# Kernel tuning notes

Hardware: AMD Instinct MI355X
Metric: run time of the kernel (lower is better)

The kernel has to match this reference:

```python
import jax, jax.numpy as jnp
import numpy as np

EPS_SQRT = 1e-9
EPS_NORM = 1e-12


def setup_inputs() -> dict:
    key = jax.random.key(0)
    k1, k2 = jax.random.split(key)
    shape = (32, 112, 112, 128)  # B, H, W, C
    left = jax.random.normal(k1, shape, dtype=jnp.float32)
    right = jax.random.normal(k2, shape, dtype=jnp.float32)
    return {"left": left, "right": right}


def reference(left, right):
    B, H, W, C = left.shape
    # reshape to [B, H*W, C] and contract over the spatial dim -> [B, C, C]
    l = left.reshape(B, H * W, C)
    r = right.reshape(B, H * W, C)
    dotted = jnp.einsum('bxc,bxd->bcd', l, r)  # batched outer-product pooling
    flat = dotted.reshape(B, C * C)
    # signed square root
    sqrted = jnp.sign(flat) * jnp.sqrt(jnp.abs(flat) + EPS_SQRT)
    # L2 normalize over the flattened bilinear vector (tf.math.l2_normalize)
    sumsq = jnp.sum(jnp.square(sqrted), axis=-1, keepdims=True)
    normed = sqrted * jax.lax.rsqrt(jnp.maximum(sumsq, EPS_NORM))
    return normed
```

## Files before the change

kernel.cpp:

```cpp
#include <hip/hip_runtime.h>
#include <hip/hip_bf16.h>


#define NK      16
#define KC      784
#define KSTEPS  49
#define BATCH   32
#define CDIM    128
#define XDIM    12544

typedef __bf16 bf16x8 __attribute__((ext_vector_type(8)));
typedef float  f32x16 __attribute__((ext_vector_type(16)));
typedef float  f32x4  __attribute__((ext_vector_type(4)));

__device__ float g_part[(size_t)NK * BATCH * CDIM * CDIM];
__device__ float g_ssq[BATCH * 8];

__global__ __launch_bounds__(512, 4)
void bcnn_gemm_kernel(const float* __restrict__ L, const float* __restrict__ R) {
  const int chunk = blockIdx.x;
  const int b     = blockIdx.y;
  const int t     = threadIdx.x;
  const int l     = t & 63;
  const int w     = t >> 6;
  const int wr    = w >> 2;
  const int wc    = w & 3;
  const int lc    = l & 31;
  const int h     = l >> 5;

  __shared__ __bf16 at_hi[2048];
  __shared__ __bf16 at_lo[2048];
  __shared__ __bf16 bt_hi[2048];
  __shared__ __bf16 bt_lo[2048];

  const int trow = t >> 5;
  const int tc4  = (t & 31) << 2;
  const int fx   = t & 7;
  const int hh   = trow >> 3;
  const int klow = trow & 7;

  int eoff[4];
#pragma unroll
  for (int j = 0; j < 4; ++j)
    eoff[j] = (((tc4 << 1) + (((j << 1) + hh) ^ fx)) << 3) + klow;

  const size_t gbase = ((size_t)b * XDIM + (size_t)chunk * KC + trow) * CDIM + tc4;
  const float* Lp = L + gbase;
  const float* Rp = R + gbase;

  const int cA0 = wr * 64 + lc;
  const int cA1 = cA0 + 32;
  const int dB  = wc * 32 + lc;
  const int offA0 = ((2 * cA0 + h) ^ ((cA0 >> 2) & 7)) << 3;
  const int offA1 = ((2 * cA1 + h) ^ ((cA1 >> 2) & 7)) << 3;
  const int offB  = ((2 * dB  + h) ^ ((dB  >> 2) & 7)) << 3;

  f32x16 acc0 = {};
  f32x16 acc1 = {};

  f32x4 lv = *(const f32x4*)Lp;
  f32x4 rv = *(const f32x4*)Rp;

  for (int s = 0; s < KSTEPS; ++s) {
    Lp += 16 * CDIM;
    Rp += 16 * CDIM;
    const float* Lpn = (s < KSTEPS - 1) ? Lp : L;
    const float* Rpn = (s < KSTEPS - 1) ? Rp : R;
    f32x4 lvn = *(const f32x4*)Lpn;
    f32x4 rvn = *(const f32x4*)Rpn;

    __syncthreads();
#pragma unroll
    for (int j = 0; j < 4; ++j) {
      float fl = lv[j];
      __bf16 lh = (__bf16)fl;
      __bf16 ll = (__bf16)(fl - (float)lh);
      at_hi[eoff[j]] = lh;
      at_lo[eoff[j]] = ll;
      float fr = rv[j];
      __bf16 rh = (__bf16)fr;
      __bf16 rl = (__bf16)(fr - (float)rh);
      bt_hi[eoff[j]] = rh;
      bt_lo[eoff[j]] = rl;
    }
    __syncthreads();

    bf16x8 ah0 = *(bf16x8*)&at_hi[offA0];
    bf16x8 al0 = *(bf16x8*)&at_lo[offA0];
    bf16x8 ah1 = *(bf16x8*)&at_hi[offA1];
    bf16x8 al1 = *(bf16x8*)&at_lo[offA1];
    bf16x8 bh  = *(bf16x8*)&bt_hi[offB];
    bf16x8 bl  = *(bf16x8*)&bt_lo[offB];

    acc0 = __builtin_amdgcn_mfma_f32_32x32x16_bf16(ah0, bh, acc0, 0, 0, 0);
    acc1 = __builtin_amdgcn_mfma_f32_32x32x16_bf16(ah1, bh, acc1, 0, 0, 0);
    acc0 = __builtin_amdgcn_mfma_f32_32x32x16_bf16(ah0, bl, acc0, 0, 0, 0);
    acc1 = __builtin_amdgcn_mfma_f32_32x32x16_bf16(ah1, bl, acc1, 0, 0, 0);
    acc0 = __builtin_amdgcn_mfma_f32_32x32x16_bf16(al0, bh, acc0, 0, 0, 0);
    acc1 = __builtin_amdgcn_mfma_f32_32x32x16_bf16(al1, bh, acc1, 0, 0, 0);

    lv = lvn;
    rv = rvn;
  }

  float* outp = g_part + (((size_t)chunk * BATCH + b) << 14);
#pragma unroll
  for (int r = 0; r < 16; ++r) {
    const int row = (r & 3) + ((r >> 2) << 3) + (h << 2);
    outp[(size_t)(wr * 64 + row) * CDIM + (wc * 32 + lc)]      = acc0[r];
    outp[(size_t)(wr * 64 + 32 + row) * CDIM + (wc * 32 + lc)] = acc1[r];
  }
}

__global__ void bcnn_sqrt_kernel(float* __restrict__ out) {
  const int b   = blockIdx.y;
  const int seg = blockIdx.x;
  const int t   = threadIdx.x;
  const int base = seg * 2048;

  float s[8];
  float ss = 0.f;
#pragma unroll
  for (int j = 0; j < 8; ++j) {
    const int idx = base + t + (j << 8);
    float v = 0.f;
#pragma unroll
    for (int ch = 0; ch < NK; ++ch)
      v += g_part[(((size_t)ch * BATCH + b) << 14) + idx];
    float a  = sqrtf(fabsf(v) + 1e-9f);
    float sg = (v > 0.f) ? 1.f : ((v < 0.f) ? -1.f : 0.f);
    float sv = sg * a;
    s[j] = sv;
    ss += sv * sv;
    out[((size_t)b << 14) + idx] = sv;
  }

#pragma unroll
  for (int o = 32; o > 0; o >>= 1) ss += __shfl_down(ss, o, 64);
  __shared__ float red[4];
  const int lane = t & 63, wid = t >> 6;
  if (lane == 0) red[wid] = ss;
  __syncthreads();
  if (t == 0) g_ssq[b * 8 + seg] = red[0] + red[1] + red[2] + red[3];
}

__global__ void bcnn_scale_kernel(float* __restrict__ out) {
  const int b   = blockIdx.y;
  const int seg = blockIdx.x;
  const int t   = threadIdx.x;

  float tot = 0.f;
#pragma unroll
  for (int i = 0; i < 8; ++i) tot += g_ssq[b * 8 + i];
  const float scale = rsqrtf(fmaxf(tot, 1e-12f));

  const size_t base = ((size_t)b << 14) + seg * 2048 + t;
#pragma unroll
  for (int j = 0; j < 8; ++j) out[base + ((size_t)j << 8)] *= scale;
}

extern "C" void kernel_launch(void* const* d_in, const int* in_sizes, int n_in,
                              void* d_out, int out_size, void* d_ws, size_t ws_size,
                              hipStream_t stream) {
  const float* L = (const float*)d_in[0];
  const float* R = (const float*)d_in[1];
  float* out = (float*)d_out;

  dim3 g1(NK, BATCH);
  bcnn_gemm_kernel<<<g1, 512, 0, stream>>>(L, R);

  dim3 g2(8, BATCH);
  bcnn_sqrt_kernel<<<g2, 256, 0, stream>>>(out);
  bcnn_scale_kernel<<<g2, 256, 0, stream>>>(out);
}
```

Before: 99.24 us.

## Deepen GEMM K-tile to 32, repack hi/lo split, increase split-K, vectorize epilogue

The GEMM kernel now processes 32 rows of the spatial dimension per barrier pair instead of 16. It splits the spatial dimension into 28 chunks instead of 16. Each thread loads 8 strided floats and packs the bf16 hi/lo pairs with integer rounding and byte-perm into 128-bit shared stores under a new swizzle. The goal is to halve the barriers and shared-store instructions per MFMA and to raise block count across CUs. In exchange the occupancy hint drops, more per-thread registers are used, and the partial buffer grows, so the reduction kernel reads more data. The reduction and scale kernels are changed to float4 accesses over 16 segments per batch.

```diff
diff --git a/kernel.cpp b/kernel.cpp
--- a/kernel.cpp
+++ b/kernel.cpp
@@ -2,21 +2,41 @@
 #include <hip/hip_bf16.h>
 
 
-#define NK      16
-#define KC      784
-#define KSTEPS  49
+#define NK      28
+#define KC      448
+#define BK      32
+#define NSTEP   14
 #define BATCH   32
 #define CDIM    128
 #define XDIM    12544
 
 typedef __bf16 bf16x8 __attribute__((ext_vector_type(8)));
 typedef float  f32x16 __attribute__((ext_vector_type(16)));
-typedef float  f32x4  __attribute__((ext_vector_type(4)));
 
 __device__ float g_part[(size_t)NK * BATCH * CDIM * CDIM];
-__device__ float g_ssq[BATCH * 8];
+__device__ float g_ssq[BATCH * 16];
 
-__global__ __launch_bounds__(512, 4)
+__device__ __forceinline__ void split_pack(const float* f, uint4& hi, uint4& lo) {
+  uint xh[8]; uint xl[8];
+#pragma unroll
+  for (int i = 0; i < 8; ++i) {
+    uint u = __float_as_uint(f[i]);
+    uint r = u + 0x7FFFu + ((u >> 16) & 1u);
+    xh[i] = r;
+    float hif = __uint_as_float(r & 0xFFFF0000u);
+    xl[i] = __float_as_uint(f[i] - hif);
+  }
+  hi.x = __builtin_amdgcn_perm(xh[1], xh[0], 0x07060302u);
+  hi.y = __builtin_amdgcn_perm(xh[3], xh[2], 0x07060302u);
+  hi.z = __builtin_amdgcn_perm(xh[5], xh[4], 0x07060302u);
+  hi.w = __builtin_amdgcn_perm(xh[7], xh[6], 0x07060302u);
+  lo.x = __builtin_amdgcn_perm(xl[1], xl[0], 0x07060302u);
+  lo.y = __builtin_amdgcn_perm(xl[3], xl[2], 0x07060302u);
+  lo.z = __builtin_amdgcn_perm(xl[5], xl[4], 0x07060302u);
+  lo.w = __builtin_amdgcn_perm(xl[7], xl[6], 0x07060302u);
+}
+
+__global__ __launch_bounds__(512, 2)
 void bcnn_gemm_kernel(const float* __restrict__ L, const float* __restrict__ R) {
   const int chunk = blockIdx.x;
   const int b     = blockIdx.y;
@@ -26,87 +46,72 @@
   const int wr    = w >> 2;
   const int wc    = w & 3;
   const int lc    = l & 31;
-  const int h     = l >> 5;
+  const int hh    = l >> 5;
 
-  __shared__ __bf16 at_hi[2048];
-  __shared__ __bf16 at_lo[2048];
-  __shared__ __bf16 bt_hi[2048];
-  __shared__ __bf16 bt_lo[2048];
+  __shared__ uint4 sAhi[512];
+  __shared__ uint4 sAlo[512];
+  __shared__ uint4 sBhi[512];
+  __shared__ uint4 sBlo[512];
 
-  const int trow = t >> 5;
-  const int tc4  = (t & 31) << 2;
-  const int fx   = t & 7;
-  const int hh   = trow >> 3;
-  const int klow = trow & 7;
+  const int sc = t & 127;
+  const int sh = t >> 7;
+  const int wu = ((sc << 2) + sh) ^ ((sc >> 1) & 7);
 
-  int eoff[4];
-#pragma unroll
-  for (int j = 0; j < 4; ++j)
-    eoff[j] = (((tc4 << 1) + (((j << 1) + hh) ^ fx)) << 3) + klow;
-
-  const size_t gbase = ((size_t)b * XDIM + (size_t)chunk * KC + trow) * CDIM + tc4;
-  const float* Lp = L + gbase;
-  const float* Rp = R + gbase;
+  const size_t gofs = ((size_t)b * XDIM + (size_t)chunk * KC + sh * 8) * CDIM + sc;
+  const float* Lp = L + gofs;
+  const float* Rp = R + gofs;
 
   const int cA0 = wr * 64 + lc;
   const int cA1 = cA0 + 32;
   const int dB  = wc * 32 + lc;
-  const int offA0 = ((2 * cA0 + h) ^ ((cA0 >> 2) & 7)) << 3;
-  const int offA1 = ((2 * cA1 + h) ^ ((cA1 >> 2) & 7)) << 3;
-  const int offB  = ((2 * dB  + h) ^ ((dB  >> 2) & 7)) << 3;
+  const int uA0 = ((cA0 << 2) + hh) ^ ((cA0 >> 1) & 7);
+  const int uA1 = ((cA1 << 2) + hh) ^ ((cA1 >> 1) & 7);
+  const int uB  = ((dB  << 2) + hh) ^ ((dB  >> 1) & 7);
 
   f32x16 acc0 = {};
   f32x16 acc1 = {};
 
-  f32x4 lv = *(const f32x4*)Lp;
-  f32x4 rv = *(const f32x4*)Rp;
+  float fl[8], fr[8];
+#pragma unroll
+  for (int i = 0; i < 8; ++i) { fl[i] = Lp[i * CDIM]; fr[i] = Rp[i * CDIM]; }
 
-  for (int s = 0; s < KSTEPS; ++s) {
-    Lp += 16 * CDIM;
-    Rp += 16 * CDIM;
-    const float* Lpn = (s < KSTEPS - 1) ? Lp : L;
-    const float* Rpn = (s < KSTEPS - 1) ? Rp : R;
-    f32x4 lvn = *(const f32x4*)Lpn;
-    f32x4 rvn = *(const f32x4*)Rpn;
+  for (int s = 0; s < NSTEP; ++s) {
+    __syncthreads();
+    uint4 h4, l4;
+    split_pack(fl, h4, l4);
+    sAhi[wu] = h4; sAlo[wu] = l4;
+    split_pack(fr, h4, l4);
+    sBhi[wu] = h4; sBlo[wu] = l4;
+
+    Lp = (s + 1 < NSTEP) ? Lp + BK * CDIM : L;
+    Rp = (s + 1 < NSTEP) ? Rp + BK * CDIM : R;
+#pragma unroll
+    for (int i = 0; i < 8; ++i) { fl[i] = Lp[i * CDIM]; fr[i] = Rp[i * CDIM]; }
 
     __syncthreads();
+
 #pragma unroll
-    for (int j = 0; j < 4; ++j) {
-      float fl = lv[j];
-      __bf16 lh = (__bf16)fl;
-      __bf16 ll = (__bf16)(fl - (float)lh);
-      at_hi[eoff[j]] = lh;
-      at_lo[eoff[j]] = ll;
-      float fr = rv[j];
-      __bf16 rh = (__bf16)fr;
-      __bf16 rl = (__bf16)(fr - (float)rh);
-      bt_hi[eoff[j]] = rh;
-      bt_lo[eoff[j]] = rl;
+    for (int ss = 0; ss < 2; ++ss) {
+      const int x = ss << 1;
+      bf16x8 ah0 = *(const bf16x8*)&sAhi[uA0 ^ x];
+      bf16x8 al0 = *(const bf16x8*)&sAlo[uA0 ^ x];
+      bf16x8 ah1 = *(const bf16x8*)&sAhi[uA1 ^ x];
+      bf16x8 al1 = *(const bf16x8*)&sAlo[uA1 ^ x];
+      bf16x8 bh  = *(const bf16x8*)&sBhi[uB  ^ x];
+      bf16x8 bl  = *(const bf16x8*)&sBlo[uB  ^ x];
+      acc0 = __builtin_amdgcn_mfma_f32_32x32x16_bf16(ah0, bh, acc0, 0, 0, 0);
+      acc1 = __builtin_amdgcn_mfma_f32_32x32x16_bf16(ah1, bh, acc1, 0, 0, 0);
+      acc0 = __builtin_amdgcn_mfma_f32_32x32x16_bf16(ah0, bl, acc0, 0, 0, 0);
+      acc1 = __builtin_amdgcn_mfma_f32_32x32x16_bf16(ah1, bl, acc1, 0, 0, 0);
+      acc0 = __builtin_amdgcn_mfma_f32_32x32x16_bf16(al0, bh, acc0, 0, 0, 0);
+      acc1 = __builtin_amdgcn_mfma_f32_32x32x16_bf16(al1, bh, acc1, 0, 0, 0);
     }
-    __syncthreads();
-
-    bf16x8 ah0 = *(bf16x8*)&at_hi[offA0];
-    bf16x8 al0 = *(bf16x8*)&at_lo[offA0];
-    bf16x8 ah1 = *(bf16x8*)&at_hi[offA1];
-    bf16x8 al1 = *(bf16x8*)&at_lo[offA1];
-    bf16x8 bh  = *(bf16x8*)&bt_hi[offB];
-    bf16x8 bl  = *(bf16x8*)&bt_lo[offB];
-
-    acc0 = __builtin_amdgcn_mfma_f32_32x32x16_bf16(ah0, bh, acc0, 0, 0, 0);
-    acc1 = __builtin_amdgcn_mfma_f32_32x32x16_bf16(ah1, bh, acc1, 0, 0, 0);
-    acc0 = __builtin_amdgcn_mfma_f32_32x32x16_bf16(ah0, bl, acc0, 0, 0, 0);
-    acc1 = __builtin_amdgcn_mfma_f32_32x32x16_bf16(ah1, bl, acc1, 0, 0, 0);
-    acc0 = __builtin_amdgcn_mfma_f32_32x32x16_bf16(al0, bh, acc0, 0, 0, 0);
-    acc1 = __builtin_amdgcn_mfma_f32_32x32x16_bf16(al1, bh, acc1, 0, 0, 0);
-
-    lv = lvn;
-    rv = rvn;
   }
 
   float* outp = g_part + (((size_t)chunk * BATCH + b) << 14);
 #pragma unroll
   for (int r = 0; r < 16; ++r) {
-    const int row = (r & 3) + ((r >> 2) << 3) + (h << 2);
+    const int row = (r & 3) + ((r >> 2) << 3) + (hh << 2);
     outp[(size_t)(wr * 64 + row) * CDIM + (wc * 32 + lc)]      = acc0[r];
     outp[(size_t)(wr * 64 + 32 + row) * CDIM + (wc * 32 + lc)] = acc1[r];
   }
@@ -116,32 +121,31 @@
   const int b   = blockIdx.y;
   const int seg = blockIdx.x;
   const int t   = threadIdx.x;
-  const int base = seg * 2048;
+  const int idx = seg * 1024 + t * 4;
 
-  float s[8];
-  float ss = 0.f;
+  float4 v = {0.f, 0.f, 0.f, 0.f};
 #pragma unroll
-  for (int j = 0; j < 8; ++j) {
-    const int idx = base + t + (j << 8);
-    float v = 0.f;
-#pragma unroll
-    for (int ch = 0; ch < NK; ++ch)
-      v += g_part[(((size_t)ch * BATCH + b) << 14) + idx];
-    float a  = sqrtf(fabsf(v) + 1e-9f);
-    float sg = (v > 0.f) ? 1.f : ((v < 0.f) ? -1.f : 0.f);
-    float sv = sg * a;
-    s[j] = sv;
-    ss += sv * sv;
-    out[((size_t)b << 14) + idx] = sv;
+  for (int ch = 0; ch < NK; ++ch) {
+    const float4 p = *(const float4*)&g_part[(((size_t)ch * BATCH + b) << 14) + idx];
+    v.x += p.x; v.y += p.y; v.z += p.z; v.w += p.w;
   }
+  float4 sv;
+  {
+    float a;
+    a = sqrtf(fabsf(v.x) + 1e-9f); sv.x = (v.x > 0.f) ? a : ((v.x < 0.f) ? -a : 0.f);
+    a = sqrtf(fabsf(v.y) + 1e-9f); sv.y = (v.y > 0.f) ? a : ((v.y < 0.f) ? -a : 0.f);
+    a = sqrtf(fabsf(v.z) + 1e-9f); sv.z = (v.z > 0.f) ? a : ((v.z < 0.f) ? -a : 0.f);
+    a = sqrtf(fabsf(v.w) + 1e-9f); sv.w = (v.w > 0.f) ? a : ((v.w < 0.f) ? -a : 0.f);
+  }
+  *(float4*)&out[((size_t)b << 14) + idx] = sv;
 
+  float ss = sv.x * sv.x + sv.y * sv.y + sv.z * sv.z + sv.w * sv.w;
 #pragma unroll
   for (int o = 32; o > 0; o >>= 1) ss += __shfl_down(ss, o, 64);
   __shared__ float red[4];
-  const int lane = t & 63, wid = t >> 6;
-  if (lane == 0) red[wid] = ss;
+  if ((t & 63) == 0) red[t >> 6] = ss;
   __syncthreads();
-  if (t == 0) g_ssq[b * 8 + seg] = red[0] + red[1] + red[2] + red[3];
+  if (t == 0) g_ssq[b * 16 + seg] = red[0] + red[1] + red[2] + red[3];
 }
 
 __global__ void bcnn_scale_kernel(float* __restrict__ out) {
@@ -151,12 +155,13 @@
 
   float tot = 0.f;
 #pragma unroll
-  for (int i = 0; i < 8; ++i) tot += g_ssq[b * 8 + i];
+  for (int i = 0; i < 16; ++i) tot += g_ssq[b * 16 + i];
   const float scale = rsqrtf(fmaxf(tot, 1e-12f));
 
-  const size_t base = ((size_t)b << 14) + seg * 2048 + t;
-#pragma unroll
-  for (int j = 0; j < 8; ++j) out[base + ((size_t)j << 8)] *= scale;
+  const size_t base = ((size_t)b << 14) + seg * 1024 + t * 4;
+  float4 v = *(float4*)&out[base];
+  v.x *= scale; v.y *= scale; v.z *= scale; v.w *= scale;
+  *(float4*)&out[base] = v;
 }
 
 extern "C" void kernel_launch(void* const* d_in, const int* in_sizes, int n_in,
@@ -169,7 +174,7 @@
   dim3 g1(NK, BATCH);
   bcnn_gemm_kernel<<<g1, 512, 0, stream>>>(L, R);
 
-  dim3 g2(8, BATCH);
+  dim3 g2(16, BATCH);
   bcnn_sqrt_kernel<<<g2, 256, 0, stream>>>(out);
   bcnn_scale_kernel<<<g2, 256, 0, stream>>>(out);
 }
```

Result: slower. 106.1 us (+6.9%).
